# Kernel optimization log

Measured on AMD Instinct MI355X. Metric: run time of the kernel, lower is better.

Reference implementation:

```python
import jax, jax.numpy as jnp
import numpy as np

B, T, H, K = 256, 1024, 12, 6
EPS = 1e-5


def _lstm_layer(x, Wih, Whh, bih, bhh):
    # x: [B, T, H]; torch gate order i, f, g, o
    b = bih + bhh

    def step(carry, xt):
        h, c = carry
        gates = xt @ Wih.T + h @ Whh.T + b
        i, f, g, o = jnp.split(gates, 4, axis=-1)
        c = jax.nn.sigmoid(f) * c + jax.nn.sigmoid(i) * jnp.tanh(g)
        h = jax.nn.sigmoid(o) * jnp.tanh(c)
        return (h, c), h

    h0 = jnp.zeros((x.shape[0], H), x.dtype)
    (_, _), ys = jax.lax.scan(step, (h0, h0), jnp.swapaxes(x, 0, 1))
    return jnp.swapaxes(ys, 0, 1)


def _bn_per_step(x, gamma, beta):
    # BatchNorm1d applied independently at each timestep (training mode):
    # normalize over the batch axis for each (t, channel).
    mu = jnp.mean(x, axis=0, keepdims=True)
    var = jnp.mean((x - mu) ** 2, axis=0, keepdims=True)  # biased, as torch BN
    return gamma * (x - mu) * jax.lax.rsqrt(var + EPS) + beta


def setup_inputs() -> dict:
    key = jax.random.key(0)
    ks = jax.random.split(key, 12)
    s = 1.0 / np.sqrt(H)
    return {
        "mfcc": jax.random.normal(ks[0], (B, T, H), jnp.float32),
        "Wih": jax.random.uniform(ks[1], (3, 4 * H, H), jnp.float32, -s, s),
        "Whh": jax.random.uniform(ks[2], (3, 4 * H, H), jnp.float32, -s, s),
        "bih": jax.random.uniform(ks[3], (3, 4 * H), jnp.float32, -s, s),
        "bhh": jax.random.uniform(ks[4], (3, 4 * H), jnp.float32, -s, s),
        "fc1_w": jax.random.normal(ks[5], (64, H), jnp.float32) * 0.1,
        "fc1_b": jnp.zeros((64,), jnp.float32),
        "bn1_g": jnp.ones((64,), jnp.float32),
        "bn1_b": jnp.zeros((64,), jnp.float32),
        "fc2_w": jax.random.normal(ks[6], (128, 64), jnp.float32) * 0.1,
        "fc2_b": jnp.zeros((128,), jnp.float32),
        "bn2_g": jnp.ones((128,), jnp.float32),
        "bn2_b": jnp.zeros((128,), jnp.float32),
        "fc3_w": jax.random.normal(ks[7], (K, 128), jnp.float32) * 0.1,
        "fc3_b": jnp.zeros((K,), jnp.float32),
        "WI": jax.random.normal(ks[8], (K, H, H), jnp.float32) * 0.01,
    }


def reference(mfcc, Wih, Whh, bih, bhh, fc1_w, fc1_b, bn1_g, bn1_b,
              fc2_w, fc2_b, bn2_g, bn2_b, fc3_w, fc3_b, WI):
    # 3-layer LSTM, input/hidden = 12
    x = mfcc
    for l in range(3):
        x = _lstm_layer(x, Wih[l], Whh[l], bih[l], bhh[l])

    # per-timestep MLP with per-timestep BatchNorm (training-mode stats)
    h = jnp.einsum('bth,oh->bto', x, fc1_w) + fc1_b
    h = jax.nn.relu(_bn_per_step(h, bn1_g, bn1_b))
    h = jnp.einsum('bth,oh->bto', h, fc2_w) + fc2_b
    h = jax.nn.relu(_bn_per_step(h, bn2_g, bn2_b))
    lambs = jnp.einsum('bth,kh->btk', h, fc3_w) + fc3_b  # [B, T, K]

    # out[b,t] = mfcc[b,t] @ (I + sum_k lambs[b,t,k] * WI[k])
    #          = mfcc[b,t] + sum_k lambs[b,t,k] * (mfcc[b,t] @ WI[k])
    proj = jnp.einsum('btd,kde->btke', mfcc, WI)  # [B, T, K, 12]
    outs = mfcc + jnp.einsum('btk,btke->bte', lambs, proj)
    return outs[:, None, :, :]  # [B, 1, T, 12]
```

## Files before the change

kernel.cpp:

```cpp
#include <hip/hip_runtime.h>

#define T_LEN 1024
#define NBATCH 256
#define HDIM 12
#define PAIR_STRIDE 12288
#define X3_TB 16

typedef __fp16 fp16x2 __attribute__((ext_vector_type(2)));

#if __has_builtin(__builtin_amdgcn_exp2f)
#define EXP2F(x) __builtin_amdgcn_exp2f(x)
#else
#define EXP2F(x) exp2f(x)
#endif
#if __has_builtin(__builtin_amdgcn_rcpf)
#define RCPF(x) __builtin_amdgcn_rcpf(x)
#else
#define RCPF(x) (1.0f / (x))
#endif

#define KSIG -1.4426950408889634f
#define KTAN -2.8853900817779268f

__device__ __forceinline__ unsigned bperm(int byteidx, unsigned v) {
#if __has_builtin(__builtin_amdgcn_ds_bpermute)
  return (unsigned)__builtin_amdgcn_ds_bpermute(byteidx, (int)v);
#else
  return (unsigned)__shfl((int)v, byteidx >> 2, 64);
#endif
}

template <int Q>
__device__ __forceinline__ float qb(float v) {
#if __has_builtin(__builtin_amdgcn_mov_dpp)
  return __int_as_float(__builtin_amdgcn_mov_dpp(__float_as_int(v), Q * 0x55, 0xF, 0xF, true));
#else
  return __shfl(v, (threadIdx.x & ~3) | Q, 64);
#endif
}

__device__ __forceinline__ float row_shr4(float v) {
#if __has_builtin(__builtin_amdgcn_mov_dpp)
  return __int_as_float(__builtin_amdgcn_mov_dpp(__float_as_int(v), 0x114, 0xF, 0xF, true));
#else
  return __shfl(v, (threadIdx.x & 63) - 4, 64);
#endif
}

__device__ __forceinline__ float h16tof(unsigned short u) {
  union { unsigned short s; _Float16 h; } c; c.s = u; return (float)c.h;
}
__device__ __forceinline__ unsigned short f16bits(float f) {
  union { unsigned short s; _Float16 h; } c; c.h = (_Float16)f; return c.s;
}
__device__ __forceinline__ float h16lo(unsigned u) {
  union { unsigned short s; _Float16 h; } c; c.s = (unsigned short)(u & 0xffffu); return (float)c.h;
}
__device__ __forceinline__ float h16hi(unsigned u) {
  union { unsigned short s; _Float16 h; } c; c.s = (unsigned short)(u >> 16); return (float)c.h;
}
__device__ __forceinline__ unsigned pk16(float a, float b) {
#if __has_builtin(__builtin_amdgcn_cvt_pkrtz)
  fp16x2 h = __builtin_amdgcn_cvt_pkrtz(a, b);
  return __builtin_bit_cast(unsigned, h);
#else
  return (unsigned)f16bits(a) | ((unsigned)f16bits(b) << 16);
#endif
}

__device__ __forceinline__ float dot2acc(unsigned a, unsigned b, float c) {
#if __has_builtin(__builtin_amdgcn_fdot2)
  return __builtin_amdgcn_fdot2(__builtin_bit_cast(fp16x2, a), __builtin_bit_cast(fp16x2, b), c, false);
#else
  return fmaf(h16lo(a), h16lo(b), fmaf(h16hi(a), h16hi(b), c));
#endif
}

__device__ __forceinline__ float d3(const unsigned* w, const unsigned* h, float init) {
  float a = dot2acc(w[0], h[0], init);
  a = dot2acc(w[1], h[1], a);
  return dot2acc(w[2], h[2], a);
}

__device__ __forceinline__ float nlup(float av, float& cv, float c1, float c0) {
  float e = EXP2F(av);
  float n = fmaf(c1, RCPF(1.f + e), c0);
  float si = qb<0>(n), sf = qb<1>(n), tg = qb<2>(n), so = qb<3>(n);
  cv = fmaf(sf, cv, si * tg);
  float e2 = EXP2F(KTAN * cv);
  return so * fmaf(2.f, RCPF(1.f + e2), -1.f);
}
__device__ __forceinline__ unsigned packb(float hq, unsigned* hp) {
  float sh = row_shr4(hq);
  unsigned pkv = pk16(sh, hq);
  hp[0] = bperm(16, pkv);  hp[1] = bperm(48, pkv);  hp[2] = bperm(80, pkv);
  hp[3] = bperm(112, pkv); hp[4] = bperm(144, pkv); hp[5] = bperm(176, pkv);
  return pkv;
}

#define BARRIER_LGKM() asm volatile("s_waitcnt lgkmcnt(0)\n\ts_barrier" ::: "memory")

__global__ __launch_bounds__(64, 4) void pregate_kernel(
    const float* __restrict__ mfcc, const float* __restrict__ Wih,
    const float* __restrict__ bih, const float* __restrict__ bhh,
    const float* __restrict__ w2, const float* __restrict__ WI,
    const float* __restrict__ w1, unsigned* __restrict__ pg2,
    unsigned* __restrict__ w2pk, unsigned* __restrict__ wipk,
    unsigned* __restrict__ w1pk) {
  if (blockIdx.x >= 2048) {
    const int base = (blockIdx.x - 2048) * 64 + threadIdx.x;
    for (int i = base; i < 4096; i += 512) {
      int kp = i >> 7, c = i & 127;
      float2 v = ((const float2*)w2)[c * 32 + kp];
      w2pk[i] = pk16(v.x, v.y);
    }
    for (int i = base; i < 432; i += 512) {
      int k6 = i / 72, rem = i % 72, e = rem / 6, dp = rem % 6;
      wipk[i] = pk16(WI[k6 * 144 + (2 * dp) * HDIM + e],
                     WI[k6 * 144 + (2 * dp + 1) * HDIM + e]);
    }
    for (int i = base; i < 384; i += 512) {
      int ch = i / 6, dp = i % 6;
      float2 v = ((const float2*)w1)[ch * 6 + dp];
      w1pk[i] = pk16(v.x, v.y);
    }
    return;
  }
  const int b = blockIdx.x & 255;
  const int tc = blockIdx.x >> 8;
  const int lane = threadIdx.x;
  const int j = lane >> 2, q = lane & 3;
  const int jj = (j < HDIM) ? j : (HDIM - 1);
  const int g = q * HDIM + jj;
  const float kqv = (q == 2) ? KTAN : KSIG;
  float w[HDIM];
#pragma unroll
  for (int m = 0; m < HDIM; ++m) w[m] = kqv * Wih[g * HDIM + m];
  const float bias = kqv * (bih[g] + bhh[g]);
  const bool wr = (lane < 48);
  const float* xb = mfcc + (b * T_LEN + tc * 128) * HDIM;
  unsigned* out = pg2 + (unsigned)(tc * 64 * NBATCH + b) * 48 + lane;
  for (int tp = 0; tp < 64; ++tp) {
    float a0 = bias, a1 = bias;
#pragma unroll
    for (int d = 0; d < HDIM; ++d) {
      a0 = fmaf(w[d], xb[d], a0);
      a1 = fmaf(w[d], xb[HDIM + d], a1);
    }
    if (wr) *out = pk16(a0, a1);
    xb += 2 * HDIM;
    out += PAIR_STRIDE;
  }
}

__global__ __launch_bounds__(192, 1) void lstm3_kernel(
    const unsigned* __restrict__ pg2,
    const float* __restrict__ Wih, const float* __restrict__ Whh,
    const float* __restrict__ bih, const float* __restrict__ bhh,
    unsigned short* __restrict__ x3) {
  __shared__ __align__(16) unsigned ldsb[192];
  const int b = blockIdx.x;
  const int tid = threadIdx.x;
  const int wid = tid >> 6;
  const int lane = tid & 63;
  const int j = lane >> 2, q = lane & 3;
  const int jj = (j < HDIM) ? j : (HDIM - 1);
  const int g = q * HDIM + jj;
  const float kqv = (q == 2) ? KTAN : KSIG;
  const float c1c = (q == 2) ? 2.0f : 1.0f;
  const float c0c = (q == 2) ? -1.0f : 0.0f;

  const int row = (wid * 48 + g) * HDIM;
  unsigned wihp[6], whhp[6];
#pragma unroll
  for (int m = 0; m < 6; ++m) {
    wihp[m] = pk16(kqv * Wih[row + 2 * m], kqv * Wih[row + 2 * m + 1]);
    whhp[m] = pk16(kqv * Whh[row + 2 * m], kqv * Whh[row + 2 * m + 1]);
  }
  const float biasw = kqv * (bih[wid * 48 + g] + bhh[wid * 48 + g]);

  float cv = 0.f;
  unsigned hown[6] = {0, 0, 0, 0, 0, 0};

  const int grpi = lane >> 3;
  const bool upper = (lane & 7) >= 4;
  const int wlayer = (wid == 0) ? 0 : 32;
  const int woff = (upper && grpi < 6) ? (wlayer + grpi) : 64;

  const int lane_src = (lane < 48) ? lane : (44 + (lane & 3));
  const char* pgbase = (const char*)(pg2 + (unsigned)b * 48);
  const unsigned PGB = PAIR_STRIDE * 4;
  const unsigned PGLIM = 513u * PGB;
  unsigned Q20 = 0, Q21 = 0, Q30 = 0, Q31 = 0, Q00 = 0, Q01 = 0, Q10 = 0, Q11 = 0;
  unsigned pg_upos = 0;
  if (wid == 0) {
    Q00 = *(const unsigned*)(pgbase + 0 * PGB + lane_src * 4);
    Q01 = *(const unsigned*)(pgbase + 1 * PGB + lane_src * 4);
    Q10 = *(const unsigned*)(pgbase + 2 * PGB + lane_src * 4);
    Q11 = *(const unsigned*)(pgbase + 3 * PGB + lane_src * 4);
    Q20 = *(const unsigned*)(pgbase + 4 * PGB + lane_src * 4);
    Q21 = *(const unsigned*)(pgbase + 5 * PGB + lane_src * 4);
    Q30 = *(const unsigned*)(pgbase + 6 * PGB + lane_src * 4);
    Q31 = *(const unsigned*)(pgbase + 7 * PGB + lane_src * 4);
    pg_upos = 8u * PGB;
  }

  char* x3b = (char*)(x3 + (unsigned)b * X3_TB);
  const int x3_loff = ((j & 1) && j < HDIM) ? (j - 1) * 2 : ((j < HDIM) ? 24 : 28);
  unsigned x3_upos = 0;
  const unsigned X3STEP = NBATCH * X3_TB * 2;

  auto l0_ss = [&](int par, unsigned pa, unsigned pb) {
    const int wb = par * 96;
    const float pgf[4] = {h16lo(pa), h16hi(pa), h16lo(pb), h16hi(pb)};
#pragma unroll
    for (int st = 0; st < 4; ++st) {
      float a = d3(whhp, hown, pgf[st]) + d3(whhp + 3, hown + 3, 0.f);
      float hq = nlup(a, cv, c1c, c0c);
      unsigned pkv = packb(hq, hown);
      ldsb[wb + woff + st * 8] = pkv;
    }
  };
  auto l1_ss = [&](int par) {
    const unsigned* rb = ldsb + (par ^ 1) * 96;
    unsigned hin[4][6];
#pragma unroll
    for (int st = 0; st < 4; ++st) {
      uint4 A = *(const uint4*)(rb + st * 8);
      uint2 B = *(const uint2*)(rb + st * 8 + 4);
      hin[st][0] = A.x; hin[st][1] = A.y; hin[st][2] = A.z;
      hin[st][3] = A.w; hin[st][4] = B.x; hin[st][5] = B.y;
    }
    const int wb = par * 96;
#pragma unroll
    for (int st = 0; st < 4; ++st) {
      float a = (d3(wihp, hin[st], biasw) + d3(wihp + 3, hin[st] + 3, 0.f)) +
                (d3(whhp, hown, 0.f) + d3(whhp + 3, hown + 3, 0.f));
      float hq = nlup(a, cv, c1c, c0c);
      unsigned pkv = packb(hq, hown);
      ldsb[wb + woff + st * 8] = pkv;
    }
  };
  auto l2_ss = [&](int par) {
    const unsigned* rb = ldsb + (par ^ 1) * 96 + 32;
    unsigned hin[4][6];
#pragma unroll
    for (int st = 0; st < 4; ++st) {
      uint4 A = *(const uint4*)(rb + st * 8);
      uint2 B = *(const uint2*)(rb + st * 8 + 4);
      hin[st][0] = A.x; hin[st][1] = A.y; hin[st][2] = A.z;
      hin[st][3] = A.w; hin[st][4] = B.x; hin[st][5] = B.y;
    }
#pragma unroll
    for (int st = 0; st < 4; ++st) {
      float a = (d3(wihp, hin[st], biasw) + d3(wihp + 3, hin[st] + 3, 0.f)) +
                (d3(whhp, hown, 0.f) + d3(whhp + 3, hown + 3, 0.f));
      float hq = nlup(a, cv, c1c, c0c);
      unsigned pkv = packb(hq, hown);
      *(unsigned*)(x3b + x3_upos + st * X3STEP + x3_loff) = pkv;
    }
    x3_upos += 4 * X3STEP;
  };

  if (wid == 0) l0_ss(0, Q00, Q01);
  BARRIER_LGKM();
  if (wid == 0) l0_ss(1, Q10, Q11);
  else if (wid == 1) l1_ss(1);
  BARRIER_LGKM();
  for (int i = 0; i < 127; ++i) {
    unsigned n00 = 0, n01 = 0, n10 = 0, n11 = 0;
    if (wid == 0) {
      unsigned o0 = pg_upos,            o1 = pg_upos + PGB;
      unsigned o2 = pg_upos + 2 * PGB,  o3 = pg_upos + 3 * PGB;
      o0 = o0 > PGLIM ? PGLIM : o0; o1 = o1 > PGLIM ? PGLIM : o1;
      o2 = o2 > PGLIM ? PGLIM : o2; o3 = o3 > PGLIM ? PGLIM : o3;
      n00 = *(const unsigned*)(pgbase + o0 + lane_src * 4);
      n01 = *(const unsigned*)(pgbase + o1 + lane_src * 4);
      n10 = *(const unsigned*)(pgbase + o2 + lane_src * 4);
      n11 = *(const unsigned*)(pgbase + o3 + lane_src * 4);
      pg_upos += 4 * PGB;
      l0_ss(0, Q20, Q21);
    } else if (wid == 1) {
      l1_ss(0);
    } else {
      l2_ss(0);
    }
    BARRIER_LGKM();
    if (wid == 0) l0_ss(1, Q30, Q31);
    else if (wid == 1) l1_ss(1);
    else l2_ss(1);
    BARRIER_LGKM();
    if (wid == 0) { Q20 = n00; Q21 = n01; Q30 = n10; Q31 = n11; }
  }
  if (wid == 1) l1_ss(0);
  else if (wid == 2) l2_ss(0);
  BARRIER_LGKM();
  if (wid == 2) l2_ss(1);
}

__global__ __launch_bounds__(256, 2) void mlp_out_kernel(
    const unsigned short* __restrict__ x3, const float* __restrict__ mfcc,
    const unsigned* __restrict__ w1pk, const float* __restrict__ g1,
    const float* __restrict__ be1, const unsigned* __restrict__ w2pk,
    const float* __restrict__ g2, const float* __restrict__ be2,
    const float* __restrict__ w3, const float* __restrict__ b3,
    const unsigned* __restrict__ wipk, float* __restrict__ outp) {
  __shared__ __align__(16) unsigned char smem[53952];
  unsigned* h1p = (unsigned*)smem;
  unsigned* w2p = (unsigned*)(smem + 32768);
  float* p3 = (float*)smem;
  float* stp = (float*)(smem + 49152);
  float* scsh = (float*)(smem + 51200);
  unsigned* wis = (unsigned*)(smem + 52224);

  const int t = blockIdx.x;
  const int tid = threadIdx.x;

  for (int i = tid; i < 1024; i += 256)
    ((uint4*)w2p)[i] = ((const uint4*)w2pk)[i];
  for (int i = tid; i < 432; i += 256) wis[i] = wipk[i];

  {
    const unsigned short* xp = x3 + t * (NBATCH * X3_TB) + tid * X3_TB;
    uint2 u0 = ((const uint2*)xp)[0];
    uint2 u1 = ((const uint2*)xp)[1];
    uint2 u2 = ((const uint2*)xp)[2];
    const unsigned u[6] = {u0.x, u0.y, u1.x, u1.y, u2.x, u2.y};
#pragma unroll 4
    for (int kp = 0; kp < 32; ++kp) {
      const unsigned* wp = w1pk + kp * 12;
      float a0 = dot2acc(wp[0], u[0], 0.f);
      float a1 = dot2acc(wp[6], u[0], 0.f);
#pragma unroll
      for (int dp = 1; dp < 6; ++dp) {
        a0 = dot2acc(wp[dp], u[dp], a0);
        a1 = dot2acc(wp[6 + dp], u[dp], a1);
      }
      h1p[kp * 256 + tid] = pk16(a0, a1);
    }
  }
  __syncthreads();

  {
    const int kp = tid & 31, seg = tid >> 5;
    const uint4* rp = (const uint4*)(h1p + kp * 256 + seg * 32);
    float sl = 0.f, sh = 0.f, ql = 0.f, qh = 0.f;
#pragma unroll
    for (int i = 0; i < 8; ++i) {
      uint4 v = rp[(i + kp) & 7];
      float f0 = h16lo(v.x), f1 = h16hi(v.x), f2 = h16lo(v.y), f3 = h16hi(v.y);
      float f4 = h16lo(v.z), f5 = h16hi(v.z), f6 = h16lo(v.w), f7 = h16hi(v.w);
      sl += (f0 + f2) + (f4 + f6);
      sh += (f1 + f3) + (f5 + f7);
      ql = fmaf(f0, f0, ql); ql = fmaf(f2, f2, ql); ql = fmaf(f4, f4, ql); ql = fmaf(f6, f6, ql);
      qh = fmaf(f1, f1, qh); qh = fmaf(f3, f3, qh); qh = fmaf(f5, f5, qh); qh = fmaf(f7, f7, qh);
    }
    sl += __shfl_xor(sl, 32, 64); sh += __shfl_xor(sh, 32, 64);
    ql += __shfl_xor(ql, 32, 64); qh += __shfl_xor(qh, 32, 64);
    if ((tid & 63) < 32) {
      float* sp = stp + kp * 16 + (tid >> 6) * 4;
      sp[0] = sl; sp[1] = sh; sp[2] = ql; sp[3] = qh;
    }
  }
  __syncthreads();
  if (tid < 64) {
    const int kp = tid >> 1, par = tid & 1;
    float s = 0.f, qq = 0.f;
#pragma unroll
    for (int w = 0; w < 4; ++w) {
      s += stp[kp * 16 + w * 4 + par];
      qq += stp[kp * 16 + w * 4 + 2 + par];
    }
    const int ch = 2 * kp + par;
    float mu = s * (1.f / 256.f);
    float var = fmaf(-mu, mu, qq * (1.f / 256.f));
    float sc = g1[ch] * rsqrtf(var + 1e-5f);
    scsh[ch * 2] = sc;
    scsh[ch * 2 + 1] = fmaf(-sc, mu, be1[ch]);
  }
  __syncthreads();
  {
    unsigned* cp = h1p + tid;
#pragma unroll 8
    for (int kp = 0; kp < 32; ++kp) {
      unsigned v = cp[kp * 256];
      float fl = fmaxf(fmaf(scsh[kp * 4 + 0], h16lo(v), scsh[kp * 4 + 1]), 0.f);
      float fh = fmaxf(fmaf(scsh[kp * 4 + 2], h16hi(v), scsh[kp * 4 + 3]), 0.f);
      cp[kp * 256] = pk16(fl, fh);
    }
  }
  __syncthreads();

  const int tb = tid & 31, tc2 = tid >> 5;
  const int b0 = tb * 8, cc0 = tc2 * 16;
  float acc[8][16];
#pragma unroll
  for (int bi = 0; bi < 8; ++bi)
#pragma unroll
    for (int ci = 0; ci < 16; ++ci) acc[bi][ci] = 0.f;

  for (int kp = 0; kp < 32; ++kp) {
    const unsigned* hrow = h1p + kp * 256 + b0;
    uint4 a01 = ((const uint4*)hrow)[0];
    uint4 a23 = ((const uint4*)hrow)[1];
    const unsigned ap[8] = {a01.x, a01.y, a01.z, a01.w, a23.x, a23.y, a23.z, a23.w};
    const unsigned* wrow = w2p + kp * 128 + cc0;
#pragma unroll
    for (int wq = 0; wq < 4; ++wq) {
      uint4 wv = ((const uint4*)wrow)[wq];
      const unsigned ww[4] = {wv.x, wv.y, wv.z, wv.w};
#pragma unroll
      for (int bi = 0; bi < 8; ++bi)
#pragma unroll
        for (int cj = 0; cj < 4; ++cj)
          acc[bi][wq * 4 + cj] = dot2acc(ap[bi], ww[cj], acc[bi][wq * 4 + cj]);
    }
  }

  {
    float sv[16], qv[16];
#pragma unroll
    for (int ci = 0; ci < 16; ++ci) {
      float s = 0.f, sq = 0.f;
#pragma unroll
      for (int bi = 0; bi < 8; ++bi) {
        s += acc[bi][ci];
        sq = fmaf(acc[bi][ci], acc[bi][ci], sq);
      }
      sv[ci] = s; qv[ci] = sq;
    }
#pragma unroll
    for (int m = 1; m <= 16; m <<= 1) {
#pragma unroll
      for (int ci = 0; ci < 16; ++ci) {
        sv[ci] += __shfl_xor(sv[ci], m, 64);
        qv[ci] += __shfl_xor(qv[ci], m, 64);
      }
    }
    if (tb == 0) {
#pragma unroll
      for (int ci = 0; ci < 16; ++ci) {
        stp[(cc0 + ci) * 2] = sv[ci];
        stp[(cc0 + ci) * 2 + 1] = qv[ci];
      }
    }
  }
  __syncthreads();
  if (tid < 128) {
    float mu = stp[tid * 2] * (1.f / 256.f);
    float var = fmaf(-mu, mu, stp[tid * 2 + 1] * (1.f / 256.f));
    float sc = g2[tid] * rsqrtf(var + 1e-5f);
    scsh[tid * 2] = sc;
    scsh[tid * 2 + 1] = fmaf(-sc, mu, be2[tid]);
  }
  __syncthreads();

  {
    float lam[8][6];
#pragma unroll
    for (int bi = 0; bi < 8; ++bi)
#pragma unroll
      for (int k6 = 0; k6 < 6; ++k6) lam[bi][k6] = 0.f;
#pragma unroll
    for (int ci = 0; ci < 16; ++ci) {
      const float sc = scsh[(cc0 + ci) * 2], shv = scsh[(cc0 + ci) * 2 + 1];
      float wv6[6];
#pragma unroll
      for (int k6 = 0; k6 < 6; ++k6) wv6[k6] = w3[k6 * 128 + cc0 + ci];
#pragma unroll
      for (int bi = 0; bi < 8; ++bi) {
        float v = fmaxf(fmaf(sc, acc[bi][ci], shv), 0.f);
#pragma unroll
        for (int k6 = 0; k6 < 6; ++k6)
          lam[bi][k6] = fmaf(v, wv6[k6], lam[bi][k6]);
      }
    }
#pragma unroll
    for (int bi = 0; bi < 8; ++bi)
#pragma unroll
      for (int k6 = 0; k6 < 6; ++k6)
        p3[(tc2 * 256 + b0 + bi) * 6 + k6] = lam[bi][k6];
  }
  __syncthreads();

  {
    float lm[6];
#pragma unroll
    for (int k6 = 0; k6 < 6; ++k6) lm[k6] = b3[k6];
#pragma unroll
    for (int tcc = 0; tcc < 8; ++tcc)
#pragma unroll
      for (int k6 = 0; k6 < 6; ++k6) lm[k6] += p3[(tcc * 256 + tid) * 6 + k6];

    const float4* mp = (const float4*)(mfcc + (tid * T_LEN + t) * HDIM);
    float4 m0 = mp[0], m1 = mp[1], m2 = mp[2];
    const float x[HDIM] = {m0.x, m0.y, m0.z, m0.w, m1.x, m1.y,
                           m1.z, m1.w, m2.x, m2.y, m2.z, m2.w};
    unsigned xpk[6];
#pragma unroll
    for (int dp = 0; dp < 6; ++dp) xpk[dp] = pk16(x[2 * dp], x[2 * dp + 1]);
    float o[HDIM];
#pragma unroll
    for (int e = 0; e < HDIM; ++e) o[e] = x[e];
#pragma unroll
    for (int k6 = 0; k6 < 6; ++k6) {
      const unsigned* wrow = wis + k6 * 72;
#pragma unroll
      for (int e = 0; e < HDIM; ++e) {
        float s = dot2acc(xpk[0], wrow[e * 6 + 0], 0.f);
        s = dot2acc(xpk[1], wrow[e * 6 + 1], s);
        s = dot2acc(xpk[2], wrow[e * 6 + 2], s);
        s = dot2acc(xpk[3], wrow[e * 6 + 3], s);
        s = dot2acc(xpk[4], wrow[e * 6 + 4], s);
        s = dot2acc(xpk[5], wrow[e * 6 + 5], s);
        o[e] = fmaf(lm[k6], s, o[e]);
      }
    }
    float4* op4 = (float4*)(outp + (tid * T_LEN + t) * HDIM);
    op4[0] = make_float4(o[0], o[1], o[2], o[3]);
    op4[1] = make_float4(o[4], o[5], o[6], o[7]);
    op4[2] = make_float4(o[8], o[9], o[10], o[11]);
  }
}

extern "C" void kernel_launch(void* const* d_in, const int* in_sizes, int n_in,
                              void* d_out, int out_size, void* d_ws, size_t ws_size,
                              hipStream_t stream) {
  const float* mfcc = (const float*)d_in[0];
  const float* Wih = (const float*)d_in[1];
  const float* Whh = (const float*)d_in[2];
  const float* bih = (const float*)d_in[3];
  const float* bhh = (const float*)d_in[4];
  const float* w1 = (const float*)d_in[5];
  const float* g1 = (const float*)d_in[7];
  const float* be1 = (const float*)d_in[8];
  const float* w2 = (const float*)d_in[9];
  const float* g2 = (const float*)d_in[11];
  const float* be2 = (const float*)d_in[12];
  const float* w3 = (const float*)d_in[13];
  const float* b3 = (const float*)d_in[14];
  const float* WI = (const float*)d_in[15];

  unsigned* pg2 = (unsigned*)d_ws;
  unsigned short* x3 = (unsigned short*)((char*)d_ws + 25264128);
  unsigned* w2pk = (unsigned*)((char*)d_ws + 33652736);
  unsigned* wipk = (unsigned*)((char*)d_ws + 33669120);
  unsigned* w1pk = (unsigned*)((char*)d_ws + 33670848);
  float* out = (float*)d_out;

  hipLaunchKernelGGL(pregate_kernel, dim3(2056), dim3(64), 0, stream,
                     mfcc, Wih, bih, bhh, w2, WI, w1, pg2, w2pk, wipk, w1pk);
  hipLaunchKernelGGL(lstm3_kernel, dim3(NBATCH), dim3(192), 0, stream,
                     pg2, Wih, Whh, bih, bhh, x3);
  hipLaunchKernelGGL(mlp_out_kernel, dim3(T_LEN), dim3(256), 0, stream,
                     x3, mfcc, w1pk, g1, be1, w2pk, g2, be2, w3, b3, wipk, out);
}
```

Before: 255.1 us.

## Process eight timesteps per barrier stage in the wavefront-pipelined LSTM

Doubles the number of timesteps each layer's wavefront handles between block barriers from 4 to 8, halving the barrier count across the 3-layer pipeline. It enlarges the LDS handoff buffers, prefetches eight input-gate values per stage, and hoists the input-to-hidden dot products for all eight steps ahead of the serial recurrence. Only one lane per group now writes to LDS, and the others write to a dummy region. The cost is longer pipeline fill and drain, more live registers, and a larger shared buffer.

```diff
diff --git a/kernel.cpp b/kernel.cpp
--- a/kernel.cpp
+++ b/kernel.cpp
@@ -158,7 +158,7 @@
     const float* __restrict__ Wih, const float* __restrict__ Whh,
     const float* __restrict__ bih, const float* __restrict__ bhh,
     unsigned short* __restrict__ x3) {
-  __shared__ __align__(16) unsigned ldsb[192];
+  __shared__ __align__(16) unsigned ldsb[320];
   const int b = blockIdx.x;
   const int tid = threadIdx.x;
   const int wid = tid >> 6;
@@ -183,26 +183,35 @@
   unsigned hown[6] = {0, 0, 0, 0, 0, 0};
 
   const int grpi = lane >> 3;
-  const bool upper = (lane & 7) >= 4;
-  const int wlayer = (wid == 0) ? 0 : 32;
-  const int woff = (upper && grpi < 6) ? (wlayer + grpi) : 64;
+  const bool wvalid = ((lane & 7) == 7) && (grpi < 6);
+  const int wlayer = (wid == 0) ? 0 : 64;
+  const int wsl = wvalid ? (wlayer + grpi) : (256 + lane);
+  const int wst = wvalid ? 8 : 0;
 
   const int lane_src = (lane < 48) ? lane : (44 + (lane & 3));
   const char* pgbase = (const char*)(pg2 + (unsigned)b * 48);
   const unsigned PGB = PAIR_STRIDE * 4;
   const unsigned PGLIM = 513u * PGB;
-  unsigned Q20 = 0, Q21 = 0, Q30 = 0, Q31 = 0, Q00 = 0, Q01 = 0, Q10 = 0, Q11 = 0;
+  uint4 P0 = {0, 0, 0, 0}, P1 = P0, A0 = P0, A1 = P0;
   unsigned pg_upos = 0;
   if (wid == 0) {
-    Q00 = *(const unsigned*)(pgbase + 0 * PGB + lane_src * 4);
-    Q01 = *(const unsigned*)(pgbase + 1 * PGB + lane_src * 4);
-    Q10 = *(const unsigned*)(pgbase + 2 * PGB + lane_src * 4);
-    Q11 = *(const unsigned*)(pgbase + 3 * PGB + lane_src * 4);
-    Q20 = *(const unsigned*)(pgbase + 4 * PGB + lane_src * 4);
-    Q21 = *(const unsigned*)(pgbase + 5 * PGB + lane_src * 4);
-    Q30 = *(const unsigned*)(pgbase + 6 * PGB + lane_src * 4);
-    Q31 = *(const unsigned*)(pgbase + 7 * PGB + lane_src * 4);
-    pg_upos = 8u * PGB;
+    P0.x = *(const unsigned*)(pgbase + 0 * PGB + lane_src * 4);
+    P0.y = *(const unsigned*)(pgbase + 1 * PGB + lane_src * 4);
+    P0.z = *(const unsigned*)(pgbase + 2 * PGB + lane_src * 4);
+    P0.w = *(const unsigned*)(pgbase + 3 * PGB + lane_src * 4);
+    P1.x = *(const unsigned*)(pgbase + 4 * PGB + lane_src * 4);
+    P1.y = *(const unsigned*)(pgbase + 5 * PGB + lane_src * 4);
+    P1.z = *(const unsigned*)(pgbase + 6 * PGB + lane_src * 4);
+    P1.w = *(const unsigned*)(pgbase + 7 * PGB + lane_src * 4);
+    A0.x = *(const unsigned*)(pgbase + 8 * PGB + lane_src * 4);
+    A0.y = *(const unsigned*)(pgbase + 9 * PGB + lane_src * 4);
+    A0.z = *(const unsigned*)(pgbase + 10 * PGB + lane_src * 4);
+    A0.w = *(const unsigned*)(pgbase + 11 * PGB + lane_src * 4);
+    A1.x = *(const unsigned*)(pgbase + 12 * PGB + lane_src * 4);
+    A1.y = *(const unsigned*)(pgbase + 13 * PGB + lane_src * 4);
+    A1.z = *(const unsigned*)(pgbase + 14 * PGB + lane_src * 4);
+    A1.w = *(const unsigned*)(pgbase + 15 * PGB + lane_src * 4);
+    pg_upos = 16u * PGB;
   }
 
   char* x3b = (char*)(x3 + (unsigned)b * X3_TB);
@@ -210,87 +219,100 @@
   unsigned x3_upos = 0;
   const unsigned X3STEP = NBATCH * X3_TB * 2;
 
-  auto l0_ss = [&](int par, unsigned pa, unsigned pb) {
-    const int wb = par * 96;
-    const float pgf[4] = {h16lo(pa), h16hi(pa), h16lo(pb), h16hi(pb)};
-#pragma unroll
-    for (int st = 0; st < 4; ++st) {
+  auto l0_ss = [&](int par, uint4 P) {
+    const int wpb = wvalid ? par * 128 : 0;
+    const float pgf[8] = {h16lo(P.x), h16hi(P.x), h16lo(P.y), h16hi(P.y),
+                          h16lo(P.z), h16hi(P.z), h16lo(P.w), h16hi(P.w)};
+#pragma unroll
+    for (int st = 0; st < 8; ++st) {
       float a = d3(whhp, hown, pgf[st]) + d3(whhp + 3, hown + 3, 0.f);
       float hq = nlup(a, cv, c1c, c0c);
       unsigned pkv = packb(hq, hown);
-      ldsb[wb + woff + st * 8] = pkv;
+      ldsb[wpb + wsl + st * wst] = pkv;
     }
   };
   auto l1_ss = [&](int par) {
-    const unsigned* rb = ldsb + (par ^ 1) * 96;
-    unsigned hin[4][6];
-#pragma unroll
-    for (int st = 0; st < 4; ++st) {
+    const unsigned* rb = ldsb + (par ^ 1) * 128;
+    unsigned hin[8][6];
+#pragma unroll
+    for (int st = 0; st < 8; ++st) {
       uint4 A = *(const uint4*)(rb + st * 8);
       uint2 B = *(const uint2*)(rb + st * 8 + 4);
       hin[st][0] = A.x; hin[st][1] = A.y; hin[st][2] = A.z;
       hin[st][3] = A.w; hin[st][4] = B.x; hin[st][5] = B.y;
     }
-    const int wb = par * 96;
-#pragma unroll
-    for (int st = 0; st < 4; ++st) {
-      float a = (d3(wihp, hin[st], biasw) + d3(wihp + 3, hin[st] + 3, 0.f)) +
-                (d3(whhp, hown, 0.f) + d3(whhp + 3, hown + 3, 0.f));
+    float aI[8];
+#pragma unroll
+    for (int st = 0; st < 8; ++st)
+      aI[st] = d3(wihp, hin[st], biasw) + d3(wihp + 3, hin[st] + 3, 0.f);
+    const int wpb = wvalid ? par * 128 : 0;
+#pragma unroll
+    for (int st = 0; st < 8; ++st) {
+      float a = aI[st] + (d3(whhp, hown, 0.f) + d3(whhp + 3, hown + 3, 0.f));
       float hq = nlup(a, cv, c1c, c0c);
       unsigned pkv = packb(hq, hown);
-      ldsb[wb + woff + st * 8] = pkv;
+      ldsb[wpb + wsl + st * wst] = pkv;
     }
   };
   auto l2_ss = [&](int par) {
-    const unsigned* rb = ldsb + (par ^ 1) * 96 + 32;
-    unsigned hin[4][6];
-#pragma unroll
-    for (int st = 0; st < 4; ++st) {
+    const unsigned* rb = ldsb + (par ^ 1) * 128 + 64;
+    unsigned hin[8][6];
+#pragma unroll
+    for (int st = 0; st < 8; ++st) {
       uint4 A = *(const uint4*)(rb + st * 8);
       uint2 B = *(const uint2*)(rb + st * 8 + 4);
       hin[st][0] = A.x; hin[st][1] = A.y; hin[st][2] = A.z;
       hin[st][3] = A.w; hin[st][4] = B.x; hin[st][5] = B.y;
     }
-#pragma unroll
-    for (int st = 0; st < 4; ++st) {
-      float a = (d3(wihp, hin[st], biasw) + d3(wihp + 3, hin[st] + 3, 0.f)) +
-                (d3(whhp, hown, 0.f) + d3(whhp + 3, hown + 3, 0.f));
+    float aI[8];
+#pragma unroll
+    for (int st = 0; st < 8; ++st)
+      aI[st] = d3(wihp, hin[st], biasw) + d3(wihp + 3, hin[st] + 3, 0.f);
+#pragma unroll
+    for (int st = 0; st < 8; ++st) {
+      float a = aI[st] + (d3(whhp, hown, 0.f) + d3(whhp + 3, hown + 3, 0.f));
       float hq = nlup(a, cv, c1c, c0c);
       unsigned pkv = packb(hq, hown);
       *(unsigned*)(x3b + x3_upos + st * X3STEP + x3_loff) = pkv;
     }
-    x3_upos += 4 * X3STEP;
+    x3_upos += 8 * X3STEP;
   };
 
-  if (wid == 0) l0_ss(0, Q00, Q01);
+  if (wid == 0) l0_ss(0, P0);
   BARRIER_LGKM();
-  if (wid == 0) l0_ss(1, Q10, Q11);
+  if (wid == 0) l0_ss(1, P1);
   else if (wid == 1) l1_ss(1);
   BARRIER_LGKM();
-  for (int i = 0; i < 127; ++i) {
-    unsigned n00 = 0, n01 = 0, n10 = 0, n11 = 0;
+  for (int i = 0; i < 63; ++i) {
+    uint4 N0 = {0, 0, 0, 0}, N1 = N0;
     if (wid == 0) {
-      unsigned o0 = pg_upos,            o1 = pg_upos + PGB;
-      unsigned o2 = pg_upos + 2 * PGB,  o3 = pg_upos + 3 * PGB;
+      unsigned o0 = pg_upos, o1 = o0 + PGB, o2 = o0 + 2 * PGB, o3 = o0 + 3 * PGB;
+      unsigned o4 = o0 + 4 * PGB, o5 = o0 + 5 * PGB, o6 = o0 + 6 * PGB, o7 = o0 + 7 * PGB;
       o0 = o0 > PGLIM ? PGLIM : o0; o1 = o1 > PGLIM ? PGLIM : o1;
       o2 = o2 > PGLIM ? PGLIM : o2; o3 = o3 > PGLIM ? PGLIM : o3;
-      n00 = *(const unsigned*)(pgbase + o0 + lane_src * 4);
-      n01 = *(const unsigned*)(pgbase + o1 + lane_src * 4);
-      n10 = *(const unsigned*)(pgbase + o2 + lane_src * 4);
-      n11 = *(const unsigned*)(pgbase + o3 + lane_src * 4);
-      pg_upos += 4 * PGB;
-      l0_ss(0, Q20, Q21);
+      o4 = o4 > PGLIM ? PGLIM : o4; o5 = o5 > PGLIM ? PGLIM : o5;
+      o6 = o6 > PGLIM ? PGLIM : o6; o7 = o7 > PGLIM ? PGLIM : o7;
+      N0.x = *(const unsigned*)(pgbase + o0 + lane_src * 4);
+      N0.y = *(const unsigned*)(pgbase + o1 + lane_src * 4);
+      N0.z = *(const unsigned*)(pgbase + o2 + lane_src * 4);
+      N0.w = *(const unsigned*)(pgbase + o3 + lane_src * 4);
+      N1.x = *(const unsigned*)(pgbase + o4 + lane_src * 4);
+      N1.y = *(const unsigned*)(pgbase + o5 + lane_src * 4);
+      N1.z = *(const unsigned*)(pgbase + o6 + lane_src * 4);
+      N1.w = *(const unsigned*)(pgbase + o7 + lane_src * 4);
+      pg_upos += 8 * PGB;
+      l0_ss(0, A0);
     } else if (wid == 1) {
       l1_ss(0);
     } else {
       l2_ss(0);
     }
     BARRIER_LGKM();
-    if (wid == 0) l0_ss(1, Q30, Q31);
+    if (wid == 0) l0_ss(1, A1);
     else if (wid == 1) l1_ss(1);
     else l2_ss(1);
     BARRIER_LGKM();
-    if (wid == 0) { Q20 = n00; Q21 = n01; Q30 = n10; Q31 = n11; }
+    if (wid == 0) { A0 = N0; A1 = N1; }
   }
   if (wid == 1) l1_ss(0);
   else if (wid == 2) l2_ss(0);
```

Measured after the change: 235.3 us. 1.08x faster.

## Widen LSTM wavefront pipeline stage from 4 to 32 timesteps per barrier

Applied to the files above, without the earlier changes.

Each layer's wavefront now processes 32 timesteps between block barriers instead of 4, with larger LDS double buffers (512 words per parity) and a deeper prefetch of layer-0 input gates held in uint4 registers. Layers 1 and 2 precompute the input-projection dot products for 16 steps before running the serial recurrence, taking that work off the dependent chain. This cuts the barrier count per sequence about eightfold and raises ILP. The cost is much higher register pressure (32-step unrolls, 16x6 staged inputs) and a longer pipeline fill and drain across the three wavefronts.

```diff
diff --git a/kernel.cpp b/kernel.cpp
--- a/kernel.cpp
+++ b/kernel.cpp
@@ -158,7 +158,7 @@
     const float* __restrict__ Wih, const float* __restrict__ Whh,
     const float* __restrict__ bih, const float* __restrict__ bhh,
     unsigned short* __restrict__ x3) {
-  __shared__ __align__(16) unsigned ldsb[192];
+  __shared__ __align__(16) unsigned ldsb[1088];
   const int b = blockIdx.x;
   const int tid = threadIdx.x;
   const int wid = tid >> 6;
@@ -183,26 +183,35 @@
   unsigned hown[6] = {0, 0, 0, 0, 0, 0};
 
   const int grpi = lane >> 3;
-  const bool upper = (lane & 7) >= 4;
-  const int wlayer = (wid == 0) ? 0 : 32;
-  const int woff = (upper && grpi < 6) ? (wlayer + grpi) : 64;
+  const bool wvalid = ((lane & 7) == 7) && (grpi < 6);
+  const int wlayer = (wid == 0) ? 0 : 256;
+  const int wsl = wvalid ? (wlayer + grpi) : (1024 + lane);
+  const int wst = wvalid ? 8 : 0;
 
   const int lane_src = (lane < 48) ? lane : (44 + (lane & 3));
   const char* pgbase = (const char*)(pg2 + (unsigned)b * 48);
   const unsigned PGB = PAIR_STRIDE * 4;
   const unsigned PGLIM = 513u * PGB;
-  unsigned Q20 = 0, Q21 = 0, Q30 = 0, Q31 = 0, Q00 = 0, Q01 = 0, Q10 = 0, Q11 = 0;
+  uint4 P[8], A[8];
+#pragma unroll
+  for (int m = 0; m < 8; ++m) { P[m] = make_uint4(0, 0, 0, 0); A[m] = P[m]; }
   unsigned pg_upos = 0;
   if (wid == 0) {
-    Q00 = *(const unsigned*)(pgbase + 0 * PGB + lane_src * 4);
-    Q01 = *(const unsigned*)(pgbase + 1 * PGB + lane_src * 4);
-    Q10 = *(const unsigned*)(pgbase + 2 * PGB + lane_src * 4);
-    Q11 = *(const unsigned*)(pgbase + 3 * PGB + lane_src * 4);
-    Q20 = *(const unsigned*)(pgbase + 4 * PGB + lane_src * 4);
-    Q21 = *(const unsigned*)(pgbase + 5 * PGB + lane_src * 4);
-    Q30 = *(const unsigned*)(pgbase + 6 * PGB + lane_src * 4);
-    Q31 = *(const unsigned*)(pgbase + 7 * PGB + lane_src * 4);
-    pg_upos = 8u * PGB;
+#pragma unroll
+    for (int m = 0; m < 8; ++m) {
+      P[m].x = *(const unsigned*)(pgbase + (4 * m + 0) * PGB + lane_src * 4);
+      P[m].y = *(const unsigned*)(pgbase + (4 * m + 1) * PGB + lane_src * 4);
+      P[m].z = *(const unsigned*)(pgbase + (4 * m + 2) * PGB + lane_src * 4);
+      P[m].w = *(const unsigned*)(pgbase + (4 * m + 3) * PGB + lane_src * 4);
+    }
+#pragma unroll
+    for (int m = 0; m < 8; ++m) {
+      A[m].x = *(const unsigned*)(pgbase + (32 + 4 * m + 0) * PGB + lane_src * 4);
+      A[m].y = *(const unsigned*)(pgbase + (32 + 4 * m + 1) * PGB + lane_src * 4);
+      A[m].z = *(const unsigned*)(pgbase + (32 + 4 * m + 2) * PGB + lane_src * 4);
+      A[m].w = *(const unsigned*)(pgbase + (32 + 4 * m + 3) * PGB + lane_src * 4);
+    }
+    pg_upos = 64u * PGB;
   }
 
   char* x3b = (char*)(x3 + (unsigned)b * X3_TB);
@@ -210,87 +219,117 @@
   unsigned x3_upos = 0;
   const unsigned X3STEP = NBATCH * X3_TB * 2;
 
-  auto l0_ss = [&](int par, unsigned pa, unsigned pb) {
-    const int wb = par * 96;
-    const float pgf[4] = {h16lo(pa), h16hi(pa), h16lo(pb), h16hi(pb)};
-#pragma unroll
-    for (int st = 0; st < 4; ++st) {
+  auto l0_ss = [&](int par, uint4 Qa, uint4 Qb, uint4 Qc, uint4 Qd) {
+    const int wpb = wvalid ? par * 512 : 0;
+    const float pgf[32] = {
+        h16lo(Qa.x), h16hi(Qa.x), h16lo(Qa.y), h16hi(Qa.y),
+        h16lo(Qa.z), h16hi(Qa.z), h16lo(Qa.w), h16hi(Qa.w),
+        h16lo(Qb.x), h16hi(Qb.x), h16lo(Qb.y), h16hi(Qb.y),
+        h16lo(Qb.z), h16hi(Qb.z), h16lo(Qb.w), h16hi(Qb.w),
+        h16lo(Qc.x), h16hi(Qc.x), h16lo(Qc.y), h16hi(Qc.y),
+        h16lo(Qc.z), h16hi(Qc.z), h16lo(Qc.w), h16hi(Qc.w),
+        h16lo(Qd.x), h16hi(Qd.x), h16lo(Qd.y), h16hi(Qd.y),
+        h16lo(Qd.z), h16hi(Qd.z), h16lo(Qd.w), h16hi(Qd.w)};
+#pragma unroll
+    for (int st = 0; st < 32; ++st) {
       float a = d3(whhp, hown, pgf[st]) + d3(whhp + 3, hown + 3, 0.f);
       float hq = nlup(a, cv, c1c, c0c);
       unsigned pkv = packb(hq, hown);
-      ldsb[wb + woff + st * 8] = pkv;
+      ldsb[wpb + wsl + st * wst] = pkv;
     }
   };
   auto l1_ss = [&](int par) {
-    const unsigned* rb = ldsb + (par ^ 1) * 96;
-    unsigned hin[4][6];
-#pragma unroll
-    for (int st = 0; st < 4; ++st) {
-      uint4 A = *(const uint4*)(rb + st * 8);
-      uint2 B = *(const uint2*)(rb + st * 8 + 4);
-      hin[st][0] = A.x; hin[st][1] = A.y; hin[st][2] = A.z;
-      hin[st][3] = A.w; hin[st][4] = B.x; hin[st][5] = B.y;
-    }
-    const int wb = par * 96;
-#pragma unroll
-    for (int st = 0; st < 4; ++st) {
-      float a = (d3(wihp, hin[st], biasw) + d3(wihp + 3, hin[st] + 3, 0.f)) +
-                (d3(whhp, hown, 0.f) + d3(whhp + 3, hown + 3, 0.f));
-      float hq = nlup(a, cv, c1c, c0c);
-      unsigned pkv = packb(hq, hown);
-      ldsb[wb + woff + st * 8] = pkv;
+    const unsigned* rb = ldsb + (par ^ 1) * 512;
+    const int wpb = wvalid ? par * 512 : 0;
+#pragma unroll
+    for (int chk = 0; chk < 2; ++chk) {
+      unsigned hin[16][6];
+#pragma unroll
+      for (int st = 0; st < 16; ++st) {
+        uint4 Av = *(const uint4*)(rb + (chk * 16 + st) * 8);
+        uint2 Bv = *(const uint2*)(rb + (chk * 16 + st) * 8 + 4);
+        hin[st][0] = Av.x; hin[st][1] = Av.y; hin[st][2] = Av.z;
+        hin[st][3] = Av.w; hin[st][4] = Bv.x; hin[st][5] = Bv.y;
+      }
+      float aI[16];
+#pragma unroll
+      for (int st = 0; st < 16; ++st)
+        aI[st] = d3(wihp, hin[st], biasw) + d3(wihp + 3, hin[st] + 3, 0.f);
+#pragma unroll
+      for (int st = 0; st < 16; ++st) {
+        float a = aI[st] + (d3(whhp, hown, 0.f) + d3(whhp + 3, hown + 3, 0.f));
+        float hq = nlup(a, cv, c1c, c0c);
+        unsigned pkv = packb(hq, hown);
+        ldsb[wpb + wsl + (chk * 16 + st) * wst] = pkv;
+      }
     }
   };
   auto l2_ss = [&](int par) {
-    const unsigned* rb = ldsb + (par ^ 1) * 96 + 32;
-    unsigned hin[4][6];
-#pragma unroll
-    for (int st = 0; st < 4; ++st) {
-      uint4 A = *(const uint4*)(rb + st * 8);
-      uint2 B = *(const uint2*)(rb + st * 8 + 4);
-      hin[st][0] = A.x; hin[st][1] = A.y; hin[st][2] = A.z;
-      hin[st][3] = A.w; hin[st][4] = B.x; hin[st][5] = B.y;
-    }
-#pragma unroll
-    for (int st = 0; st < 4; ++st) {
-      float a = (d3(wihp, hin[st], biasw) + d3(wihp + 3, hin[st] + 3, 0.f)) +
-                (d3(whhp, hown, 0.f) + d3(whhp + 3, hown + 3, 0.f));
-      float hq = nlup(a, cv, c1c, c0c);
-      unsigned pkv = packb(hq, hown);
-      *(unsigned*)(x3b + x3_upos + st * X3STEP + x3_loff) = pkv;
-    }
-    x3_upos += 4 * X3STEP;
+    const unsigned* rb = ldsb + (par ^ 1) * 512 + 256;
+#pragma unroll
+    for (int chk = 0; chk < 2; ++chk) {
+      unsigned hin[16][6];
+#pragma unroll
+      for (int st = 0; st < 16; ++st) {
+        uint4 Av = *(const uint4*)(rb + (chk * 16 + st) * 8);
+        uint2 Bv = *(const uint2*)(rb + (chk * 16 + st) * 8 + 4);
+        hin[st][0] = Av.x; hin[st][1] = Av.y; hin[st][2] = Av.z;
+        hin[st][3] = Av.w; hin[st][4] = Bv.x; hin[st][5] = Bv.y;
+      }
+      float aI[16];
+#pragma unroll
+      for (int st = 0; st < 16; ++st)
+        aI[st] = d3(wihp, hin[st], biasw) + d3(wihp + 3, hin[st] + 3, 0.f);
+#pragma unroll
+      for (int st = 0; st < 16; ++st) {
+        float a = aI[st] + (d3(whhp, hown, 0.f) + d3(whhp + 3, hown + 3, 0.f));
+        float hq = nlup(a, cv, c1c, c0c);
+        unsigned pkv = packb(hq, hown);
+        *(unsigned*)(x3b + x3_upos + (chk * 16 + st) * X3STEP + x3_loff) = pkv;
+      }
+    }
+    x3_upos += 32 * X3STEP;
   };
 
-  if (wid == 0) l0_ss(0, Q00, Q01);
+  if (wid == 0) l0_ss(0, P[0], P[1], P[2], P[3]);
   BARRIER_LGKM();
-  if (wid == 0) l0_ss(1, Q10, Q11);
+  if (wid == 0) l0_ss(1, P[4], P[5], P[6], P[7]);
   else if (wid == 1) l1_ss(1);
   BARRIER_LGKM();
-  for (int i = 0; i < 127; ++i) {
-    unsigned n00 = 0, n01 = 0, n10 = 0, n11 = 0;
+  for (int i = 0; i < 15; ++i) {
+    uint4 N[8];
+#pragma unroll
+    for (int m = 0; m < 8; ++m) N[m] = make_uint4(0, 0, 0, 0);
     if (wid == 0) {
-      unsigned o0 = pg_upos,            o1 = pg_upos + PGB;
-      unsigned o2 = pg_upos + 2 * PGB,  o3 = pg_upos + 3 * PGB;
-      o0 = o0 > PGLIM ? PGLIM : o0; o1 = o1 > PGLIM ? PGLIM : o1;
-      o2 = o2 > PGLIM ? PGLIM : o2; o3 = o3 > PGLIM ? PGLIM : o3;
-      n00 = *(const unsigned*)(pgbase + o0 + lane_src * 4);
-      n01 = *(const unsigned*)(pgbase + o1 + lane_src * 4);
-      n10 = *(const unsigned*)(pgbase + o2 + lane_src * 4);
-      n11 = *(const unsigned*)(pgbase + o3 + lane_src * 4);
-      pg_upos += 4 * PGB;
-      l0_ss(0, Q20, Q21);
+#pragma unroll
+      for (int m = 0; m < 8; ++m) {
+        unsigned o0 = pg_upos + (4 * m + 0) * PGB;
+        unsigned o1 = pg_upos + (4 * m + 1) * PGB;
+        unsigned o2 = pg_upos + (4 * m + 2) * PGB;
+        unsigned o3 = pg_upos + (4 * m + 3) * PGB;
+        o0 = o0 > PGLIM ? PGLIM : o0; o1 = o1 > PGLIM ? PGLIM : o1;
+        o2 = o2 > PGLIM ? PGLIM : o2; o3 = o3 > PGLIM ? PGLIM : o3;
+        N[m].x = *(const unsigned*)(pgbase + o0 + lane_src * 4);
+        N[m].y = *(const unsigned*)(pgbase + o1 + lane_src * 4);
+        N[m].z = *(const unsigned*)(pgbase + o2 + lane_src * 4);
+        N[m].w = *(const unsigned*)(pgbase + o3 + lane_src * 4);
+      }
+      pg_upos += 32 * PGB;
+      l0_ss(0, A[0], A[1], A[2], A[3]);
     } else if (wid == 1) {
       l1_ss(0);
     } else {
       l2_ss(0);
     }
     BARRIER_LGKM();
-    if (wid == 0) l0_ss(1, Q30, Q31);
+    if (wid == 0) l0_ss(1, A[4], A[5], A[6], A[7]);
     else if (wid == 1) l1_ss(1);
     else l2_ss(1);
     BARRIER_LGKM();
-    if (wid == 0) { Q20 = n00; Q21 = n01; Q30 = n10; Q31 = n11; }
+    if (wid == 0) {
+#pragma unroll
+      for (int m = 0; m < 8; ++m) A[m] = N[m];
+    }
   }
   if (wid == 1) l1_ss(0);
   else if (wid == 2) l2_ss(0);
```

After: 227.7 us. 1.12x faster.
